# Performance work log

Measured on AMD Instinct MI355X. Metric: run time of the kernel, lower is better.

## Reference

```python
import jax, jax.numpy as jnp
import numpy as np

N, IN_DIM, OUT_DIM = 8192, 512, 256
ALPHA = 0.2  # LeakyReLU negative slope
MASK_VAL = -9e15


def setup_inputs() -> dict:
    key = jax.random.key(0)
    k1, k2, k3, k4 = jax.random.split(key, 4)
    inp = jax.random.normal(k1, (N, IN_DIM), dtype=jnp.float32)
    adj = jax.random.randint(k2, (N, N), 0, 2, dtype=jnp.int32)
    # xavier-ish scaled params
    weight = jax.random.normal(k3, (IN_DIM, OUT_DIM), dtype=jnp.float32) * (2.0 / (IN_DIM + OUT_DIM)) ** 0.5
    a = jax.random.normal(k4, (2 * OUT_DIM, 1), dtype=jnp.float32) * (2.0 / (2 * OUT_DIM + 1)) ** 0.5
    return {"input": inp, "adj": adj, "weight": weight, "a": a}


def reference(input, adj, weight, a):
    Wh = input @ weight                        # [N, D_out]
    Wh1 = Wh @ a[:OUT_DIM, :]                  # [N, 1]
    Wh2 = Wh @ a[OUT_DIM:, :]                  # [N, 1]
    e = Wh1 + Wh2.T                            # [N, N] broadcast additive score
    e = jnp.where(e > 0, e, ALPHA * e)         # LeakyReLU
    e = jnp.where(adj > 0, e, MASK_VAL)        # adjacency mask
    attention = jax.nn.softmax(e, axis=-1)     # [N, N]
    # dropout p=0.0 -> identity
    out = attention @ Wh                       # [N, D_out]
    return jax.nn.elu(out)
```

## Files before the change

### kernel.cpp

```cpp
#include <hip/hip_runtime.h>
#include <hip/hip_bf16.h>
#include <stdint.h>

#define NN 8192
#define DIN 512
#define DOUT 256
#define NSPLIT 8
#define STRIP (NN / NSPLIT)
#define KVBLK 64
#define NSTEP (STRIP / KVBLK)
#define LOG2E 1.4426950408889634f

typedef short short8 __attribute__((ext_vector_type(8)));
typedef float floatx4 __attribute__((ext_vector_type(4)));

__device__ __forceinline__ unsigned short f2bf_rne(float x) {
  unsigned u = __float_as_uint(x);
  u += 0x7fffu + ((u >> 16) & 1u);
  return (unsigned short)(u >> 16);
}

__device__ __forceinline__ unsigned cvt_pk_bf16(float lo, float hi) {
  unsigned r;
  asm("v_cvt_pk_bf16_f32 %0, %1, %2" : "=v"(r) : "v"(lo), "v"(hi));
  return r;
}

__global__ __launch_bounds__(256) void kt_transpose(const float* __restrict__ Wg,
                                                    unsigned short* __restrict__ WT) {
  __shared__ unsigned short sm[32][33];
  int tid = threadIdx.x;
  int bk = blockIdx.x >> 3;
  int bn = blockIdx.x & 7;
  int k0 = bk * 32, n0 = bn * 32;
  int r = tid >> 3, c4 = (tid & 7) * 4;
  const float* src = Wg + (size_t)(k0 + r) * DOUT + n0 + c4;
#pragma unroll
  for (int x = 0; x < 4; ++x) sm[r][c4 + x] = f2bf_rne(src[x]);
  __syncthreads();
  unsigned short* dst = WT + (size_t)(n0 + r) * DIN + k0 + c4;
#pragma unroll
  for (int x = 0; x < 4; ++x) dst[x] = sm[c4 + x][r];
}

__global__ __launch_bounds__(256) void kt_cvtx(const float* __restrict__ X,
                                               unsigned short* __restrict__ Xb) {
  int g = blockIdx.x * 256 + threadIdx.x;
  const float4* p = (const float4*)(X + (size_t)g * 8);
  float4 a = p[0], b = p[1];
  union { unsigned u[4]; short8 s8; } r;
  r.u[0] = cvt_pk_bf16(a.x, a.y);
  r.u[1] = cvt_pk_bf16(a.z, a.w);
  r.u[2] = cvt_pk_bf16(b.x, b.y);
  r.u[3] = cvt_pk_bf16(b.z, b.w);
  *(short8*)(Xb + (size_t)g * 8) = r.s8;
}

__global__ __launch_bounds__(256, 2) void kt_gemm1(const unsigned short* __restrict__ Xb,
                                                   const unsigned short* __restrict__ WT,
                                                   const float* __restrict__ Ab,
                                                   unsigned short* __restrict__ WhTb,
                                                   float* __restrict__ Wh1,
                                                   float* __restrict__ Wh2) {
  __shared__ __align__(16) unsigned short xs[64 * DIN];
  int tid = threadIdx.x;
  int w = tid >> 6, lane = tid & 63;
  int col = lane & 15, q = lane >> 4;
  int ib = blockIdx.x & 127;
  int db = blockIdx.x >> 7;
  int i0 = ib * 64;

  int sr = tid >> 2, sc = tid & 3, sxor = sr & 7;
  const unsigned short* gX = Xb + (size_t)(i0 + sr) * DIN + sc * 8;
  unsigned short* lX = xs + sr * DIN;
  short8 stg[8];
#pragma unroll
  for (int n = 0; n < 8; ++n) stg[n] = *(const short8*)(gX + n * 32);
#pragma unroll
  for (int n = 0; n < 8; ++n) {
    int l = sc + n * 4;
    *(short8*)(lX + ((l ^ sxor) * 8)) = stg[n];
  }
#pragma unroll
  for (int n = 8; n < 16; ++n) stg[n - 8] = *(const short8*)(gX + n * 32);
#pragma unroll
  for (int n = 8; n < 16; ++n) {
    int l = sc + n * 4;
    *(short8*)(lX + ((l ^ sxor) * 8)) = stg[n - 8];
  }

  int drow = db * 64 + w * 16 + col;
  const unsigned short* abase = WT + (size_t)drow * DIN + q * 8;
  short8 af[16];
#pragma unroll
  for (int s = 0; s < 16; ++s) af[s] = *(const short8*)(abase + s * 32);

  __syncthreads();

  floatx4 acc[4];
#pragma unroll
  for (int t = 0; t < 4; ++t) acc[t] = (floatx4)(0.0f);
  int cx = col & 7;
#pragma unroll
  for (int s = 0; s < 16; ++s) {
#pragma unroll
    for (int t = 0; t < 4; ++t) {
      short8 bf = *(const short8*)(xs + (t * 16 + col) * DIN + (((s * 4 + q) ^ cx) * 8));
      acc[t] = __builtin_amdgcn_mfma_f32_16x16x32_bf16(af[s], bf, acc[t], 0, 0, 0);
    }
  }

  int dq = db * 64 + w * 16 + q * 4;
  float a1v[4], a2v[4];
#pragma unroll
  for (int r = 0; r < 4; ++r) {
    a1v[r] = Ab[dq + r] * LOG2E;
    a2v[r] = Ab[DOUT + dq + r] * LOG2E;
  }
#pragma unroll
  for (int t = 0; t < 4; ++t) {
    floatx4 v = acc[t];
    int icol = i0 + t * 16 + col;
#pragma unroll
    for (int r = 0; r < 4; ++r)
      WhTb[((size_t)(icol >> 5) * DOUT + (dq + r)) * 32 + (icol & 31)] = f2bf_rne(v[r]);
    float p1 = v[0] * a1v[0] + v[1] * a1v[1] + v[2] * a1v[2] + v[3] * a1v[3];
    float p2 = v[0] * a2v[0] + v[1] * a2v[1] + v[2] * a2v[2] + v[3] * a2v[3];
    p1 += __shfl_xor(p1, 16);
    p1 += __shfl_xor(p1, 32);
    p2 += __shfl_xor(p2, 16);
    p2 += __shfl_xor(p2, 32);
    if (q == 0) {
      atomicAdd(&Wh1[icol], p1);
      atomicAdd(&Wh2[icol], p2);
    }
  }
}

__device__ __forceinline__ short8 build_a(int4 pa, int4 pb, float wh1, floatx4 w2a,
                                          floatx4 w2b, float& lsum) {
  int av[8] = {pa.x, pa.y, pa.z, pa.w, pb.x, pb.y, pb.z, pb.w};
  float w2[8] = {w2a[0], w2a[1], w2a[2], w2a[3], w2b[0], w2b[1], w2b[2], w2b[3]};
  float wv[8];
#pragma unroll
  for (int e = 0; e < 8; ++e) {
    float sc = wh1 + w2[e];
    sc = fmaxf(sc, 0.2f * sc);
    float ex = __builtin_amdgcn_exp2f(sc);
    wv[e] = (av[e] != 0) ? ex : 0.0f;
  }
  union { unsigned u[4]; short8 s8; } r;
#pragma unroll
  for (int p = 0; p < 4; ++p) {
    unsigned pk = cvt_pk_bf16(wv[2 * p], wv[2 * p + 1]);
    r.u[p] = pk;
    lsum += __uint_as_float(pk << 16) + __uint_as_float(pk & 0xffff0000u);
  }
  return r.s8;
}

__global__ __launch_bounds__(256, 2) void kt_attn(const int* __restrict__ adj,
                                                  const unsigned short* __restrict__ WhTb,
                                                  const float* __restrict__ Wh1,
                                                  const float* __restrict__ Wh2,
                                                  float* __restrict__ accs,
                                                  float* __restrict__ lgp) {
  __shared__ __align__(16) unsigned short tileB[2][DOUT * KVBLK];
  __shared__ __align__(16) float wh2s[STRIP];
  int tid = threadIdx.x;
  int w = tid >> 6, lane = tid & 63;
  int col = lane & 15, q = lane >> 4;
  int s = blockIdx.x & (NSPLIT - 1);
  int ib = blockIdx.x >> 3;
  int i0 = ib * 128;
  int jb = s * STRIP;

  ((float4*)wh2s)[tid] = ((const float4*)(Wh2 + jb))[tid];

  int r0 = i0 + w * 32 + col;
  float wh1r0 = Wh1[r0];
  float wh1r1 = Wh1[r0 + 16];

  const unsigned short* gW = WhTb + (size_t)(s * 32) * 8192 + tid * 8;
  int scn = tid & 3, sx = (tid >> 2) & 7;
  unsigned short* lrow0 = &tileB[0][(tid >> 2) * KVBLK];
  int wo[2];
  wo[0] = ((scn ^ sx) * 8);
  wo[1] = (((4 + scn) ^ sx) * 8);

  int ck = col & 7;
  int off0 = col * KVBLK + ((q ^ ck) * 8);
  int off1 = col * KVBLK + (((4 + q) ^ ck) * 8);
  const unsigned short* tb0 = &tileB[0][0];

  const int* aptr0 = adj + ((size_t)r0 << 13) + jb + q * 8;
  const int* aptr1 = adj + ((size_t)(r0 + 16) << 13) + jb + q * 8;

  floatx4 acc0[16], acc1[16];
#pragma unroll
  for (int t = 0; t < 16; ++t) {
    acc0[t] = (floatx4)(0.0f);
    acc1[t] = (floatx4)(0.0f);
  }
  float lp0 = 0.f, lp1 = 0.f;

  short8 st[8];
#pragma unroll
  for (int n = 0; n < 2; ++n)
#pragma unroll
    for (int m = 0; m < 4; ++m)
      st[n * 4 + m] = *(const short8*)(gW + n * 8192 + m * 2048);
  int4 aA0a = *(const int4*)aptr0;
  int4 aA0b = *(const int4*)(aptr0 + 4);
  int4 aA1a = *(const int4*)aptr1;
  int4 aA1b = *(const int4*)(aptr1 + 4);
  int4 aB0a = *(const int4*)(aptr0 + 32);
  int4 aB0b = *(const int4*)(aptr0 + 36);
  int4 aB1a = *(const int4*)(aptr1 + 32);
  int4 aB1b = *(const int4*)(aptr1 + 36);

#pragma unroll 1
  for (int k = 0; k < NSTEP; ++k) {
    int bsel = (k & 1) * (DOUT * KVBLK);
    unsigned short* lw = lrow0 + bsel;
#pragma unroll
    for (int n = 0; n < 2; ++n)
#pragma unroll
      for (int m = 0; m < 4; ++m)
        *(short8*)(lw + m * (64 * KVBLK) + wo[n]) = st[n * 4 + m];
    if (k + 1 < NSTEP) {
      const unsigned short* gs = gW + (size_t)(2 * (k + 1)) * 8192;
#pragma unroll
      for (int n = 0; n < 2; ++n)
#pragma unroll
        for (int m = 0; m < 4; ++m)
          st[n * 4 + m] = *(const short8*)(gs + n * 8192 + m * 2048);
    }
    asm volatile("s_waitcnt lgkmcnt(0)\ns_barrier" ::: "memory");
    int jl = k * KVBLK;
    {
      floatx4 w2a = *(const floatx4*)&wh2s[jl + q * 8];
      floatx4 w2b = *(const floatx4*)&wh2s[jl + q * 8 + 4];
      short8 af0 = build_a(aA0a, aA0b, wh1r0, w2a, w2b, lp0);
      short8 af1 = build_a(aA1a, aA1b, wh1r1, w2a, w2b, lp1);
      if (k + 1 < NSTEP) {
        int jn = (k + 1) * KVBLK;
        aA0a = *(const int4*)(aptr0 + jn);
        aA0b = *(const int4*)(aptr0 + jn + 4);
        aA1a = *(const int4*)(aptr1 + jn);
        aA1b = *(const int4*)(aptr1 + jn + 4);
      }
      const unsigned short* br = tb0 + bsel + off0;
#pragma unroll
      for (int h = 0; h < 4; ++h) {
        short8 bf[4];
#pragma unroll
        for (int t = 0; t < 4; ++t) bf[t] = *(const short8*)(br + (h * 4 + t) * 1024);
#pragma unroll
        for (int t = 0; t < 4; ++t) {
          acc0[h * 4 + t] =
              __builtin_amdgcn_mfma_f32_16x16x32_bf16(af0, bf[t], acc0[h * 4 + t], 0, 0, 0);
          acc1[h * 4 + t] =
              __builtin_amdgcn_mfma_f32_16x16x32_bf16(af1, bf[t], acc1[h * 4 + t], 0, 0, 0);
        }
      }
    }
    {
      floatx4 w2a = *(const floatx4*)&wh2s[jl + 32 + q * 8];
      floatx4 w2b = *(const floatx4*)&wh2s[jl + 32 + q * 8 + 4];
      short8 ag0 = build_a(aB0a, aB0b, wh1r0, w2a, w2b, lp0);
      short8 ag1 = build_a(aB1a, aB1b, wh1r1, w2a, w2b, lp1);
      if (k + 1 < NSTEP) {
        int jn = (k + 1) * KVBLK + 32;
        aB0a = *(const int4*)(aptr0 + jn);
        aB0b = *(const int4*)(aptr0 + jn + 4);
        aB1a = *(const int4*)(aptr1 + jn);
        aB1b = *(const int4*)(aptr1 + jn + 4);
      }
      const unsigned short* br = tb0 + bsel + off1;
#pragma unroll
      for (int h = 0; h < 4; ++h) {
        short8 bf[4];
#pragma unroll
        for (int t = 0; t < 4; ++t) bf[t] = *(const short8*)(br + (h * 4 + t) * 1024);
#pragma unroll
        for (int t = 0; t < 4; ++t) {
          acc0[h * 4 + t] =
              __builtin_amdgcn_mfma_f32_16x16x32_bf16(ag0, bf[t], acc0[h * 4 + t], 0, 0, 0);
          acc1[h * 4 + t] =
              __builtin_amdgcn_mfma_f32_16x16x32_bf16(ag1, bf[t], acc1[h * 4 + t], 0, 0, 0);
        }
      }
    }
  }

  lp0 += __shfl_xor(lp0, 16);
  lp0 += __shfl_xor(lp0, 32);
  lp1 += __shfl_xor(lp1, 16);
  lp1 += __shfl_xor(lp1, 32);
  if (lane < 16) {
    __builtin_nontemporal_store(lp0, &lgp[(size_t)s * NN + i0 + w * 32 + lane]);
    __builtin_nontemporal_store(lp1, &lgp[(size_t)s * NN + i0 + w * 32 + 16 + lane]);
  }
  float* slab = accs + (size_t)s * NN * DOUT;
#pragma unroll
  for (int T = 0; T < 16; ++T) {
    floatx4 v0 = acc0[T];
    floatx4 v1 = acc1[T];
    int dcol = T * 16 + col;
    int irow0 = i0 + w * 32 + q * 4;
#pragma unroll
    for (int r = 0; r < 4; ++r)
      __builtin_nontemporal_store(v0[r], &slab[(size_t)(irow0 + r) * DOUT + dcol]);
#pragma unroll
    for (int r = 0; r < 4; ++r)
      __builtin_nontemporal_store(v1[r], &slab[(size_t)(irow0 + 16 + r) * DOUT + dcol]);
  }
}

__global__ __launch_bounds__(256) void kt_merge(const float* __restrict__ accs,
                                                const float* __restrict__ lgp,
                                                float* __restrict__ out) {
  int g = blockIdx.x * 256 + threadIdx.x;
  int i = g >> 6;
  float l = 0.f;
#pragma unroll
  for (int s = 0; s < NSPLIT; ++s) l += lgp[(size_t)s * NN + i];
  float4 a = *(const float4*)(accs + (size_t)g * 4);
#pragma unroll
  for (int s = 1; s < NSPLIT; ++s) {
    float4 b = *(const float4*)(accs + (size_t)s * NN * DOUT + (size_t)g * 4);
    a.x += b.x; a.y += b.y; a.z += b.z; a.w += b.w;
  }
  float inv = 1.0f / l;
  float o[4] = {a.x * inv, a.y * inv, a.z * inv, a.w * inv};
#pragma unroll
  for (int r = 0; r < 4; ++r) o[r] = o[r] > 0.f ? o[r] : (__expf(o[r]) - 1.f);
  *(float4*)(out + (size_t)g * 4) = make_float4(o[0], o[1], o[2], o[3]);
}

extern "C" void kernel_launch(void* const* d_in, const int* in_sizes, int n_in,
                              void* d_out, int out_size, void* d_ws, size_t ws_size,
                              hipStream_t stream) {
  const float* X = (const float*)d_in[0];
  const int* adj = (const int*)d_in[1];
  const float* Wg = (const float*)d_in[2];
  const float* Ab = (const float*)d_in[3];
  float* out = (float*)d_out;

  char* ws = (char*)d_ws;
  float* accs = (float*)ws;
  unsigned short* Xb = (unsigned short*)ws;
  size_t off = (size_t)NSPLIT * NN * DOUT * 4;
  float* lgp = (float*)(ws + off);
  off += (size_t)NSPLIT * NN * 4;
  float* Wh1 = (float*)(ws + off);
  off += (size_t)NN * 4;
  float* Wh2 = (float*)(ws + off);
  off += (size_t)NN * 4;
  unsigned short* WT = (unsigned short*)(ws + off);
  off += (size_t)DOUT * DIN * 2;
  unsigned short* WhTb = (unsigned short*)(ws + off);
  off += (size_t)DOUT * NN * 2;

  hipMemsetAsync(Wh1, 0, (size_t)NN * 8, stream);
  kt_cvtx<<<2048, 256, 0, stream>>>(X, Xb);
  kt_transpose<<<128, 256, 0, stream>>>(Wg, WT);
  kt_gemm1<<<512, 256, 0, stream>>>(Xb, WT, Ab, WhTb, Wh1, Wh2);
  kt_attn<<<(NN / 128) * NSPLIT, 256, 0, stream>>>(adj, WhTb, Wh1, Wh2, accs, lgp);
  kt_merge<<<2048, 256, 0, stream>>>(accs, lgp, out);
}
```

Before: 445.2 us.

## Fuse input bf16 conversion into GEMM1 and stage Wh tiles via direct global-to-LDS loads

Drops the separate fp32-to-bf16 conversion kernel for X by converting inside the first GEMM's LDS staging, saving one launch and a round trip through global memory. It also changes the WhTb layout so that it is pre-swizzled in 32-column chunks. The attention kernel then copies B tiles straight into LDS with global_load_lds, where available, instead of staging them through registers. The swizzle is matched on both the write side and the read side. The risk is that the register-staging prefetch overlap is replaced by a barrier-based double buffer, whose async loads may not be waited on correctly.

```diff
diff --git a/kernel.cpp b/kernel.cpp
--- a/kernel.cpp
+++ b/kernel.cpp
@@ -11,6 +11,15 @@
 #define NSTEP (STRIP / KVBLK)
 #define LOG2E 1.4426950408889634f
 
+#ifdef __has_builtin
+#if __has_builtin(__builtin_amdgcn_global_load_lds)
+#define HAVE_GLL 1
+#endif
+#endif
+#ifndef HAVE_GLL
+#define HAVE_GLL 0
+#endif
+
 typedef short short8 __attribute__((ext_vector_type(8)));
 typedef float floatx4 __attribute__((ext_vector_type(4)));
 
@@ -24,6 +33,17 @@
   unsigned r;
   asm("v_cvt_pk_bf16_f32 %0, %1, %2" : "=v"(r) : "v"(lo), "v"(hi));
   return r;
+}
+
+__device__ __forceinline__ void stage16(unsigned short* lds, const unsigned short* g,
+                                        int lane) {
+#if HAVE_GLL
+  __builtin_amdgcn_global_load_lds(
+      (const __attribute__((address_space(1))) unsigned int*)(g + lane * 8),
+      (__attribute__((address_space(3))) unsigned int*)lds, 16, 0, 0);
+#else
+  *(short8*)(lds + lane * 8) = *(const short8*)(g + lane * 8);
+#endif
 }
 
 __global__ __launch_bounds__(256) void kt_transpose(const float* __restrict__ Wg,
@@ -43,20 +63,7 @@
   for (int x = 0; x < 4; ++x) dst[x] = sm[c4 + x][r];
 }
 
-__global__ __launch_bounds__(256) void kt_cvtx(const float* __restrict__ X,
-                                               unsigned short* __restrict__ Xb) {
-  int g = blockIdx.x * 256 + threadIdx.x;
-  const float4* p = (const float4*)(X + (size_t)g * 8);
-  float4 a = p[0], b = p[1];
-  union { unsigned u[4]; short8 s8; } r;
-  r.u[0] = cvt_pk_bf16(a.x, a.y);
-  r.u[1] = cvt_pk_bf16(a.z, a.w);
-  r.u[2] = cvt_pk_bf16(b.x, b.y);
-  r.u[3] = cvt_pk_bf16(b.z, b.w);
-  *(short8*)(Xb + (size_t)g * 8) = r.s8;
-}
-
-__global__ __launch_bounds__(256, 2) void kt_gemm1(const unsigned short* __restrict__ Xb,
+__global__ __launch_bounds__(256, 2) void kt_gemm1(const float* __restrict__ X,
                                                    const unsigned short* __restrict__ WT,
                                                    const float* __restrict__ Ab,
                                                    unsigned short* __restrict__ WhTb,
@@ -71,22 +78,26 @@
   int i0 = ib * 64;
 
   int sr = tid >> 2, sc = tid & 3, sxor = sr & 7;
-  const unsigned short* gX = Xb + (size_t)(i0 + sr) * DIN + sc * 8;
+  const float* gX = X + (size_t)(i0 + sr) * DIN + sc * 8;
   unsigned short* lX = xs + sr * DIN;
-  short8 stg[8];
-#pragma unroll
-  for (int n = 0; n < 8; ++n) stg[n] = *(const short8*)(gX + n * 32);
-#pragma unroll
-  for (int n = 0; n < 8; ++n) {
-    int l = sc + n * 4;
-    *(short8*)(lX + ((l ^ sxor) * 8)) = stg[n];
-  }
-#pragma unroll
-  for (int n = 8; n < 16; ++n) stg[n - 8] = *(const short8*)(gX + n * 32);
-#pragma unroll
-  for (int n = 8; n < 16; ++n) {
-    int l = sc + n * 4;
-    *(short8*)(lX + ((l ^ sxor) * 8)) = stg[n - 8];
+#pragma unroll
+  for (int n = 0; n < 16; n += 4) {
+    float4 fa[4], fb[4];
+#pragma unroll
+    for (int j2 = 0; j2 < 4; ++j2) {
+      fa[j2] = *(const float4*)(gX + (n + j2) * 32);
+      fb[j2] = *(const float4*)(gX + (n + j2) * 32 + 4);
+    }
+#pragma unroll
+    for (int j2 = 0; j2 < 4; ++j2) {
+      union { unsigned u[4]; short8 s8; } rr;
+      rr.u[0] = cvt_pk_bf16(fa[j2].x, fa[j2].y);
+      rr.u[1] = cvt_pk_bf16(fa[j2].z, fa[j2].w);
+      rr.u[2] = cvt_pk_bf16(fb[j2].x, fb[j2].y);
+      rr.u[3] = cvt_pk_bf16(fb[j2].z, fb[j2].w);
+      int l = sc + (n + j2) * 4;
+      *(short8*)(lX + ((l ^ sxor) * 8)) = rr.s8;
+    }
   }
 
   int drow = db * 64 + w * 16 + col;
@@ -121,9 +132,13 @@
   for (int t = 0; t < 4; ++t) {
     floatx4 v = acc[t];
     int icol = i0 + t * 16 + col;
-#pragma unroll
-    for (int r = 0; r < 4; ++r)
-      WhTb[((size_t)(icol >> 5) * DOUT + (dq + r)) * 32 + (icol & 31)] = f2bf_rne(v[r]);
+    int g = icol >> 5, c = (icol >> 3) & 3, e = icol & 7;
+#pragma unroll
+    for (int r = 0; r < 4; ++r) {
+      int d = dq + r;
+      WhTb[(size_t)g * 8192 + (size_t)d * 32 + ((c ^ ((d >> 1) & 3)) * 8) + e] =
+          f2bf_rne(v[r]);
+    }
     float p1 = v[0] * a1v[0] + v[1] * a1v[1] + v[2] * a1v[2] + v[3] * a1v[3];
     float p2 = v[0] * a2v[0] + v[1] * a2v[1] + v[2] * a2v[2] + v[3] * a2v[3];
     p1 += __shfl_xor(p1, 16);
@@ -165,7 +180,7 @@
                                                   const float* __restrict__ Wh2,
                                                   float* __restrict__ accs,
                                                   float* __restrict__ lgp) {
-  __shared__ __align__(16) unsigned short tileB[2][DOUT * KVBLK];
+  __shared__ __align__(16) unsigned short tileB[2 * 2 * 8192];
   __shared__ __align__(16) float wh2s[STRIP];
   int tid = threadIdx.x;
   int w = tid >> 6, lane = tid & 63;
@@ -181,17 +196,12 @@
   float wh1r0 = Wh1[r0];
   float wh1r1 = Wh1[r0 + 16];
 
-  const unsigned short* gW = WhTb + (size_t)(s * 32) * 8192 + tid * 8;
-  int scn = tid & 3, sx = (tid >> 2) & 7;
-  unsigned short* lrow0 = &tileB[0][(tid >> 2) * KVBLK];
-  int wo[2];
-  wo[0] = ((scn ^ sx) * 8);
-  wo[1] = (((4 + scn) ^ sx) * 8);
-
-  int ck = col & 7;
-  int off0 = col * KVBLK + ((q ^ ck) * 8);
-  int off1 = col * KVBLK + (((4 + q) ^ ck) * 8);
-  const unsigned short* tb0 = &tileB[0][0];
+  const unsigned short* gW = WhTb + (size_t)(s * 32) * 8192;
+  int wq = w * 4;
+
+  int kq = (col >> 1) & 3;
+  int off0 = col * 32 + ((q ^ kq) * 8);
+  const unsigned short* tb0 = &tileB[0];
 
   const int* aptr0 = adj + ((size_t)r0 << 13) + jb + q * 8;
   const int* aptr1 = adj + ((size_t)(r0 + 16) << 13) + jb + q * 8;
@@ -204,12 +214,11 @@
   }
   float lp0 = 0.f, lp1 = 0.f;
 
-  short8 st[8];
 #pragma unroll
   for (int n = 0; n < 2; ++n)
 #pragma unroll
     for (int m = 0; m < 4; ++m)
-      st[n * 4 + m] = *(const short8*)(gW + n * 8192 + m * 2048);
+      stage16(&tileB[n * 8192 + (wq + m) * 512], gW + n * 8192 + (wq + m) * 512, lane);
   int4 aA0a = *(const int4*)aptr0;
   int4 aA0b = *(const int4*)(aptr0 + 4);
   int4 aA1a = *(const int4*)aptr1;
@@ -221,22 +230,17 @@
 
 #pragma unroll 1
   for (int k = 0; k < NSTEP; ++k) {
-    int bsel = (k & 1) * (DOUT * KVBLK);
-    unsigned short* lw = lrow0 + bsel;
-#pragma unroll
-    for (int n = 0; n < 2; ++n)
-#pragma unroll
-      for (int m = 0; m < 4; ++m)
-        *(short8*)(lw + m * (64 * KVBLK) + wo[n]) = st[n * 4 + m];
+    __syncthreads();
+    int bsel = (k & 1) * 16384;
     if (k + 1 < NSTEP) {
       const unsigned short* gs = gW + (size_t)(2 * (k + 1)) * 8192;
+      unsigned short* ls = &tileB[((k + 1) & 1) * 16384];
 #pragma unroll
       for (int n = 0; n < 2; ++n)
 #pragma unroll
         for (int m = 0; m < 4; ++m)
-          st[n * 4 + m] = *(const short8*)(gs + n * 8192 + m * 2048);
-    }
-    asm volatile("s_waitcnt lgkmcnt(0)\ns_barrier" ::: "memory");
+          stage16(ls + n * 8192 + (wq + m) * 512, gs + n * 8192 + (wq + m) * 512, lane);
+    }
     int jl = k * KVBLK;
     {
       floatx4 w2a = *(const floatx4*)&wh2s[jl + q * 8];
@@ -255,7 +259,7 @@
       for (int h = 0; h < 4; ++h) {
         short8 bf[4];
 #pragma unroll
-        for (int t = 0; t < 4; ++t) bf[t] = *(const short8*)(br + (h * 4 + t) * 1024);
+        for (int t = 0; t < 4; ++t) bf[t] = *(const short8*)(br + (h * 4 + t) * 512);
 #pragma unroll
         for (int t = 0; t < 4; ++t) {
           acc0[h * 4 + t] =
@@ -277,12 +281,12 @@
         aB1a = *(const int4*)(aptr1 + jn);
         aB1b = *(const int4*)(aptr1 + jn + 4);
       }
-      const unsigned short* br = tb0 + bsel + off1;
+      const unsigned short* br = tb0 + bsel + 8192 + off0;
 #pragma unroll
       for (int h = 0; h < 4; ++h) {
         short8 bf[4];
 #pragma unroll
-        for (int t = 0; t < 4; ++t) bf[t] = *(const short8*)(br + (h * 4 + t) * 1024);
+        for (int t = 0; t < 4; ++t) bf[t] = *(const short8*)(br + (h * 4 + t) * 512);
 #pragma unroll
         for (int t = 0; t < 4; ++t) {
           acc0[h * 4 + t] =
@@ -350,7 +354,6 @@
 
   char* ws = (char*)d_ws;
   float* accs = (float*)ws;
-  unsigned short* Xb = (unsigned short*)ws;
   size_t off = (size_t)NSPLIT * NN * DOUT * 4;
   float* lgp = (float*)(ws + off);
   off += (size_t)NSPLIT * NN * 4;
@@ -364,9 +367,8 @@
   off += (size_t)DOUT * NN * 2;
 
   hipMemsetAsync(Wh1, 0, (size_t)NN * 8, stream);
-  kt_cvtx<<<2048, 256, 0, stream>>>(X, Xb);
   kt_transpose<<<128, 256, 0, stream>>>(Wg, WT);
-  kt_gemm1<<<512, 256, 0, stream>>>(Xb, WT, Ab, WhTb, Wh1, Wh2);
+  kt_gemm1<<<512, 256, 0, stream>>>(X, WT, Ab, WhTb, Wh1, Wh2);
   kt_attn<<<(NN / 128) * NSPLIT, 256, 0, stream>>>(adj, WhTb, Wh1, Wh2, accs, lgp);
   kt_merge<<<2048, 256, 0, stream>>>(accs, lgp, out);
 }
```

Result: no change. 443.4 us (-0.4%).
